# Performance work log

Hardware: AMD Instinct MI355X
Metric: run time of the kernel (lower is better)

The kernel has to match this reference:

```python
import jax, jax.numpy as jnp
import numpy as np
import math

B, H, S, DK = 2, 16, 2048, 64

def setup_inputs() -> dict:
    key = jax.random.key(0)
    kq, kk, kv, km = jax.random.split(key, 4)
    q = jax.random.normal(kq, (B, H, S, DK), dtype=jnp.float32)
    k = jax.random.normal(kk, (B, H, S, DK), dtype=jnp.float32)
    v = jax.random.normal(kv, (B, H, S, DK), dtype=jnp.float32)
    mask = jax.random.randint(km, (1, 1, S, S), 0, 2).astype(jnp.bool_)
    return {"q": q, "k": k, "v": v, "mask": mask}

def reference(q, k, v, mask):
    d_k = q.shape[-1]
    # scores: [B,H,Sq,Sk]
    scores = jnp.einsum('bhqd,bhkd->bhqk', q, k) / math.sqrt(d_k)
    scores = jnp.where(mask, jnp.float32(-1e9), scores)
    # NOTE: original uses nn.Softmax(dim=2) -> softmax over the QUERY axis
    attn = jax.nn.softmax(scores, axis=2)
    out = jnp.einsum('bhqk,bhkd->bhqd', attn, v)
    return out
```

## Files before the change

### kernel.cpp

```cpp
#include <hip/hip_runtime.h>
#include <math.h>

#define S_LEN 2048
#define NCH   32
#define N_BH  32

typedef short bf16x8 __attribute__((ext_vector_type(8)));
typedef _Float16 f16x8 __attribute__((ext_vector_type(8)));
typedef __fp16 fp16x2 __attribute__((ext_vector_type(2)));
typedef float f32x4  __attribute__((ext_vector_type(4)));
typedef unsigned short u16;
typedef unsigned short u16x8 __attribute__((ext_vector_type(8)));
typedef unsigned long long u64;

#define MFMA32(a,b,c) __builtin_amdgcn_mfma_f32_16x16x32_bf16((a),(b),(c),0,0,0)
#define MFMAH(a,b,c)  __builtin_amdgcn_mfma_f32_16x16x32_f16((a),(b),(c),0,0,0)
#define EXP2(x) __builtin_amdgcn_exp2f(x)

#define SC        0.18033688011112042f
#define MASKED_P  6.103515625e-05f

__device__ __forceinline__ u16 f2h(float x) {
  union { _Float16 h; u16 u; } v;
  v.h = (_Float16)x;
  return v.u;
}
__device__ __forceinline__ u16 f2bf_rne(float x) {
  unsigned u = __float_as_uint(x);
  return (u16)((u + 0x7FFF + ((u >> 16) & 1)) >> 16);
}
__device__ __forceinline__ void bfsplit(float x, u16& h, u16& l) {
  unsigned u = __float_as_uint(x);
  h = (u16)(u >> 16);
  float hf = __uint_as_float(u & 0xFFFF0000u);
  l = f2bf_rne(x - hf);
}

__global__ __launch_bounds__(256) void pack_mask(
    const int* __restrict__ mask, u64* __restrict__ bits) {
  const int word = blockIdx.x * 4 + (threadIdx.x >> 6);
  const int lane = threadIdx.x & 63;
  const int row = word >> 5, wc = word & 31;
  int m = mask[(size_t)row * S_LEN + wc * 64 + lane];
  u64 b = __ballot(m != 0);
  if (lane == 0) bits[word] = b;
}

__global__ __launch_bounds__(256) void prep_qk_mask(
    const float* __restrict__ Q, const float* __restrict__ K,
    const int* __restrict__ mask,
    u16* __restrict__ qf, u16* __restrict__ kf, u64* __restrict__ bits) {
  const int b = blockIdx.x;
  const int tid = threadIdx.x;
  if (b < 1024) {
    const int slot = tid & 15, r0 = tid >> 4;
    const size_t rowbase = (size_t)b * 64;
#pragma unroll
    for (int p = 0; p < 4; ++p) {
      const size_t row = rowbase + p * 16 + r0;
      const size_t dst = row * 64 + ((slot * 4) ^ (((int)row & 7) << 3));
      float4 xq = *(const float4*)(Q + row * 64 + slot * 4);
      *(ushort4*)(qf + dst) = make_ushort4(
          f2h(xq.x * SC), f2h(xq.y * SC), f2h(xq.z * SC), f2h(xq.w * SC));
      float4 xk = *(const float4*)(K + row * 64 + slot * 4);
      *(ushort4*)(kf + dst) = make_ushort4(
          f2h(xk.x), f2h(xk.y), f2h(xk.z), f2h(xk.w));
    }
  } else {
    const int word = (b - 1024) * 4 + (tid >> 6);
    const int lane = tid & 63;
    const int row = word >> 5, wc = word & 31;
    int m = mask[(size_t)row * S_LEN + wc * 64 + lane];
    u64 bb = __ballot(m != 0);
    if (lane == 0) bits[word] = bb;
  }
}

__global__ __launch_bounds__(256) void prep_w(
    const float* __restrict__ V, const float* __restrict__ part,
    u16* __restrict__ w_t) {
  __shared__ __align__(16) u16 ts[4096];
  const int tid = threadIdx.x;
  const int kc = blockIdx.x, bh = blockIdx.y;
  const int k = tid >> 2, dblk = (tid & 3) * 16;
  const size_t ko = (size_t)bh * S_LEN + kc * 64 + k;
  const float lsum = part[ko] + part[65536 + ko]
                   + part[131072 + ko] + part[196608 + ko];
  const float ilk = 1.0f / lsum;
  const float* vb = V + ko * 64 + dblk;
#pragma unroll
  for (int u = 0; u < 4; ++u) {
    float4 x = *(const float4*)(vb + u * 4);
    float xs[4] = {x.x, x.y, x.z, x.w};
#pragma unroll
    for (int e = 0; e < 4; ++e) {
      const int d = dblk + u * 4 + e;
      ts[d * 64 + (k ^ ((d & 7) << 3))] = f2h(xs[e] * ilk);
    }
  }
  __syncthreads();
  u16* dst = w_t + ((size_t)bh * NCH + kc) * 4096;
#pragma unroll
  for (int j = 0; j < 2; ++j)
    *(u16x8*)(dst + j * 2048 + tid * 8) = *(const u16x8*)(ts + j * 2048 + tid * 8);
}

__global__ __launch_bounds__(512, 4) void passA(
    const u16* __restrict__ qf, const u16* __restrict__ kf,
    const u64* __restrict__ mbits, float* __restrict__ part) {
  __shared__ __align__(16) u16 qbuf[2][4096];

  const int tid = threadIdx.x;
  const int lane = tid & 63;
  const int w = tid >> 6;
  const int c = lane & 15;
  const int g = lane >> 4;
  const int bx = blockIdx.x;
  const int bh = blockIdx.y;
  const int qp = blockIdx.z;

  const size_t bh_off = (size_t)bh * S_LEN * 64;
  const int swc = (c & 7) << 3;

  f16x8 ka[2][2];
#pragma unroll
  for (int t = 0; t < 2; ++t) {
    const int row = bx * 256 + w * 32 + t * 16 + c;
#pragma unroll
    for (int h = 0; h < 2; ++h)
      ka[t][h] = *(const f16x8*)(kf + bh_off + (size_t)row * 64
                                 + ((h * 32 + g * 8) ^ swc));
  }

  u16x8 stg = *(const u16x8*)(qf + bh_off + (size_t)(qp * 512) * 64 + tid * 8);
  *(u16x8*)(&qbuf[0][0] + tid * 8) = stg;
  __syncthreads();

  float lp[2][4] = {{0.f, 0.f, 0.f, 0.f}, {0.f, 0.f, 0.f, 0.f}};
  const int word = bx * 4 + (w >> 1);
  const int sh0 = (w & 1) * 32;

  int cur = 0;
  for (int qs = 0; qs < 8; ++qs) {
    if (qs + 1 < 8)
      stg = *(const u16x8*)(qf + bh_off
            + (size_t)(qp * 512 + (qs + 1) * 64) * 64 + tid * 8);

    const u16* qb = &qbuf[cur][0];
#pragma unroll
    for (int sub = 0; sub < 4; ++sub) {
      f16x8 fh[2];
      const int rb = sub * 1024 + c * 64;
#pragma unroll
      for (int h = 0; h < 2; ++h)
        fh[h] = *(const f16x8*)(qb + rb + ((h * 32 + g * 8) ^ swc));
      const int qrow = qp * 512 + qs * 64 + sub * 16 + c;
      const u64 mw = mbits[(size_t)qrow * NCH + word];
#pragma unroll
      for (int t = 0; t < 2; ++t) {
        f32x4 acc = {0.f, 0.f, 0.f, 0.f};
        __builtin_amdgcn_s_setprio(1);
        acc = MFMAH(ka[t][0], fh[0], acc);
        acc = MFMAH(ka[t][1], fh[1], acc);
        __builtin_amdgcn_s_setprio(0);
        const unsigned nib = (unsigned)(mw >> (sh0 + t * 16 + g * 4)) & 0xFu;
#pragma unroll
        for (int r = 0; r < 4; ++r) {
          const float tv = EXP2(acc[r]);
          lp[t][r] += ((nib >> r) & 1) ? MASKED_P : tv;
        }
      }
    }

    if (qs + 1 < 8)
      *(u16x8*)(&qbuf[cur ^ 1][0] + tid * 8) = stg;
    __syncthreads();
    cur ^= 1;
  }

#pragma unroll
  for (int off = 1; off < 16; off <<= 1)
#pragma unroll
    for (int t = 0; t < 2; ++t)
#pragma unroll
      for (int r = 0; r < 4; ++r) lp[t][r] += __shfl_xor(lp[t][r], off, 64);
  if (c == 0) {
#pragma unroll
    for (int t = 0; t < 2; ++t) {
      float4 o = {lp[t][0], lp[t][1], lp[t][2], lp[t][3]};
      *(float4*)(part + (size_t)qp * 65536 + (size_t)bh * S_LEN
                 + bx * 256 + w * 32 + t * 16 + g * 4) = o;
    }
  }
}

__global__ __launch_bounds__(256, 4) void passC(
    const u16* __restrict__ qf, const u16* __restrict__ kf,
    const u16* __restrict__ w_t, const u64* __restrict__ mbits,
    float* __restrict__ out) {
  __shared__ __align__(16) u16 sbuf[2][8192];
  __shared__ __align__(16) u16 p_s[4096];

  const int tid = threadIdx.x;
  const int lane = tid & 63;
  const int w = tid >> 6;
  const int c = lane & 15;
  const int g = lane >> 4;
  const int qc = blockIdx.x;
  const int bh = blockIdx.y;

  const size_t bh_off = (size_t)bh * S_LEN * 64;
  const u16* tb_k = kf + bh_off;
  const u16* tb_w = w_t + (size_t)bh * NCH * 4096;
  const int swc = (c & 7) << 3;

  const int qrow = qc * 64 + w * 16 + c;
  f16x8 qb_[2];
#pragma unroll
  for (int h = 0; h < 2; ++h)
    qb_[h] = *(const f16x8*)(qf + bh_off + (size_t)qrow * 64
                             + ((h * 32 + g * 8) ^ swc));

  f32x4 oacc[4];
#pragma unroll
  for (int dt = 0; dt < 4; ++dt) oacc[dt] = (f32x4){0.f, 0.f, 0.f, 0.f};

  const int pbase = w * 1024 + c * 64;
  const int so = tid * 8;

  u16x8 stg[4];
#pragma unroll
  for (int j = 0; j < 2; ++j) {
    stg[0 + j] = *(const u16x8*)(tb_k + j * 2048 + so);
    stg[2 + j] = *(const u16x8*)(tb_w + j * 2048 + so);
  }
#pragma unroll
  for (int j = 0; j < 2; ++j) {
    *(u16x8*)(&sbuf[0][0] + j * 2048 + so) = stg[0 + j];
    *(u16x8*)(&sbuf[0][0] + 4096 + j * 2048 + so) = stg[2 + j];
  }
  __syncthreads();

  int cur = 0;
  for (int kc = 0; kc < NCH; ++kc) {
    if (kc + 1 < NCH) {
      const size_t nb = (size_t)(kc + 1) * 4096;
#pragma unroll
      for (int j = 0; j < 2; ++j) {
        stg[0 + j] = *(const u16x8*)(tb_k + nb + j * 2048 + so);
        stg[2 + j] = *(const u16x8*)(tb_w + nb + j * 2048 + so);
      }
    }

    const u16* bufc = &sbuf[cur][0];
    const u64 mw = mbits[(size_t)qrow * NCH + kc];

#pragma unroll
    for (int kt = 0; kt < 4; ++kt) {
      const int kbase = (16 * kt + c) * 64;
      f16x8 ak0 = *(const f16x8*)(bufc + kbase + ((g * 8) ^ swc));
      f16x8 ak1 = *(const f16x8*)(bufc + kbase + ((32 + g * 8) ^ swc));
      f32x4 acc = {0.f, 0.f, 0.f, 0.f};
      __builtin_amdgcn_s_setprio(1);
      acc = MFMAH(ak0, qb_[0], acc);
      acc = MFMAH(ak1, qb_[1], acc);
      __builtin_amdgcn_s_setprio(0);
      const unsigned nib = (unsigned)(mw >> (kt * 16 + g * 4)) & 0xFu;
      float p[4];
#pragma unroll
      for (int r = 0; r < 4; ++r) {
        const float tv = EXP2(acc[r]);
        p[r] = ((nib >> r) & 1) ? MASKED_P : tv;
      }
      union { fp16x2 h; unsigned u; } cl, ch;
      cl.h = __builtin_amdgcn_cvt_pkrtz(p[0], p[1]);
      ch.h = __builtin_amdgcn_cvt_pkrtz(p[2], p[3]);
      *(uint2*)(p_s + pbase + ((kt * 16 + g * 4) ^ swc)) = make_uint2(cl.u, ch.u);
    }

    __builtin_amdgcn_s_setprio(1);
#pragma unroll
    for (int s2 = 0; s2 < 2; ++s2) {
      const int koff = (s2 * 32 + g * 8) ^ swc;
      f16x8 pb8 = *(const f16x8*)(p_s + pbase + koff);
#pragma unroll
      for (int dt = 0; dt < 4; ++dt) {
        f16x8 av = *(const f16x8*)(bufc + 4096 + (16 * dt + c) * 64 + koff);
        oacc[dt] = MFMAH(av, pb8, oacc[dt]);
      }
    }
    __builtin_amdgcn_s_setprio(0);

    if (kc + 1 < NCH) {
      u16* bufn = &sbuf[cur ^ 1][0];
#pragma unroll
      for (int j = 0; j < 2; ++j) {
        *(u16x8*)(bufn + j * 2048 + so) = stg[0 + j];
        *(u16x8*)(bufn + 4096 + j * 2048 + so) = stg[2 + j];
      }
    }
    __syncthreads();
    cur ^= 1;
  }

  float* ob = out + (bh_off + (size_t)qrow * 64);
#pragma unroll
  for (int dt = 0; dt < 4; ++dt) {
    float4 o = {oacc[dt][0], oacc[dt][1], oacc[dt][2], oacc[dt][3]};
    *(float4*)(ob + dt * 16 + g * 4) = o;
  }
}

__global__ __launch_bounds__(256) void passA_colsum(
    const float* __restrict__ Q, const float* __restrict__ K,
    const u64* __restrict__ mbits, float* __restrict__ il_out) {
  const int tid = threadIdx.x;
  const int lane = tid & 63;
  const int w = tid >> 6;
  const int c = lane & 15;
  const int g = lane >> 4;
  const int kc = blockIdx.x;
  const int bh = blockIdx.y;

  const float* Qb = Q + (size_t)bh * S_LEN * 64;
  const float* Kb = K + (size_t)bh * S_LEN * 64;

  bf16x8 kah[2], kal[2];
  {
    const int krow = kc * 64 + w * 16 + c;
#pragma unroll
    for (int h = 0; h < 2; ++h) {
      const float* src = Kb + (size_t)krow * 64 + h * 32 + g * 8;
      float4 x = *(const float4*)(src);
      float4 y = *(const float4*)(src + 4);
      float xs[8] = {x.x, x.y, x.z, x.w, y.x, y.y, y.z, y.w};
#pragma unroll
      for (int e = 0; e < 8; ++e) {
        u16 hh, ll; bfsplit(xs[e], hh, ll);
        kah[h][e] = (short)hh; kal[h][e] = (short)ll;
      }
    }
  }

  float lp[4] = {0.f, 0.f, 0.f, 0.f};
  const int shift = w * 16 + g * 4;

  for (int qs = 0; qs < S_LEN / 16; ++qs) {
    const int qrow = qs * 16 + c;
    bf16x8 qbh_[2], qbl_[2];
#pragma unroll
    for (int h = 0; h < 2; ++h) {
      const float* src = Qb + (size_t)qrow * 64 + h * 32 + g * 8;
      float4 x = *(const float4*)(src);
      float4 y = *(const float4*)(src + 4);
      float xs[8] = {x.x, x.y, x.z, x.w, y.x, y.y, y.z, y.w};
#pragma unroll
      for (int e = 0; e < 8; ++e) {
        u16 hh, ll; bfsplit(xs[e] * SC, hh, ll);
        qbh_[h][e] = (short)hh; qbl_[h][e] = (short)ll;
      }
    }
    f32x4 acc = {0.f, 0.f, 0.f, 0.f};
#pragma unroll
    for (int h = 0; h < 2; ++h) {
      acc = MFMA32(kah[h], qbh_[h], acc);
      acc = MFMA32(kal[h], qbh_[h], acc);
      acc = MFMA32(kah[h], qbl_[h], acc);
    }
    u64 mw = mbits[(size_t)qrow * NCH + kc];
    unsigned nib = (unsigned)(mw >> shift) & 0xFu;
#pragma unroll
    for (int r = 0; r < 4; ++r) {
      float s = ((nib >> r) & 1) ? -30.0f : acc[r];
      lp[r] += exp2f(s);
    }
  }
#pragma unroll
  for (int off = 1; off < 16; off <<= 1)
#pragma unroll
    for (int r = 0; r < 4; ++r) lp[r] += __shfl_xor(lp[r], off, 64);
  if (c == 0) {
    float4 o = {1.f / lp[0], 1.f / lp[1], 1.f / lp[2], 1.f / lp[3]};
    *(float4*)(il_out + (size_t)bh * S_LEN + kc * 64 + w * 16 + g * 4) = o;
  }
}

__global__ __launch_bounds__(256) void passC_out(
    const float* __restrict__ Q, const float* __restrict__ K,
    const float* __restrict__ V, const u64* __restrict__ mbits,
    const float* __restrict__ il_in, float* __restrict__ out) {
  __shared__ u16 kh_s[4096];
  __shared__ u16 kl_s[4096];
  __shared__ u16 vt_s[4096];
  __shared__ u16 p_s[4096];

  const int tid = threadIdx.x;
  const int lane = tid & 63;
  const int w = tid >> 6;
  const int c = lane & 15;
  const int g = lane >> 4;
  const int qc = blockIdx.x;
  const int bh = blockIdx.y;

  const float* Qb = Q + (size_t)bh * S_LEN * 64;
  const float* Kb = K + (size_t)bh * S_LEN * 64;
  const float* Vb = V + (size_t)bh * S_LEN * 64;

  bf16x8 qbh_[2], qbl_[2];
  {
    const int qrow = qc * 64 + w * 16 + c;
#pragma unroll
    for (int h = 0; h < 2; ++h) {
      const float* src = Qb + (size_t)qrow * 64 + h * 32 + g * 8;
      float4 x = *(const float4*)(src);
      float4 y = *(const float4*)(src + 4);
      float xs[8] = {x.x, x.y, x.z, x.w, y.x, y.y, y.z, y.w};
#pragma unroll
      for (int e = 0; e < 8; ++e) {
        u16 hh, ll; bfsplit(xs[e] * SC, hh, ll);
        qbh_[h][e] = (short)hh; qbl_[h][e] = (short)ll;
      }
    }
  }

  f32x4 oacc[4];
#pragma unroll
  for (int dt = 0; dt < 4; ++dt) oacc[dt] = (f32x4){0.f, 0.f, 0.f, 0.f};

  const int slot = tid & 15, r0 = tid >> 4;
  const int kv = tid & 63, dblk = tid >> 6;
  const int swc = (c & 7) << 3;
  const int pbase = w * 1024 + c * 64;

  for (int kc = 0; kc < NCH; ++kc) {
    __syncthreads();
#pragma unroll
    for (int p = 0; p < 4; ++p) {
      const int row = p * 16 + r0;
      float4 kx = *(const float4*)(Kb + (size_t)(kc * 64 + row) * 64 + slot * 4);
      float xs[4] = {kx.x, kx.y, kx.z, kx.w};
      u16 ha[4], la[4];
#pragma unroll
      for (int e = 0; e < 4; ++e) bfsplit(xs[e], ha[e], la[e]);
      const int idx = row * 64 + ((slot * 4) ^ ((row & 7) << 3));
      *(ushort4*)(kh_s + idx) = make_ushort4(ha[0], ha[1], ha[2], ha[3]);
      *(ushort4*)(kl_s + idx) = make_ushort4(la[0], la[1], la[2], la[3]);
    }
    {
      const float ilk = il_in[(size_t)bh * S_LEN + kc * 64 + kv];
#pragma unroll
      for (int u = 0; u < 4; ++u) {
        float4 vv = *(const float4*)(Vb + (size_t)(kc * 64 + kv) * 64 + dblk * 16 + u * 4);
        float xs[4] = {vv.x, vv.y, vv.z, vv.w};
#pragma unroll
        for (int e = 0; e < 4; ++e) {
          const int d = dblk * 16 + u * 4 + e;
          vt_s[d * 64 + (kv ^ ((d & 7) << 3))] = f2bf_rne(xs[e] * ilk);
        }
      }
    }
    __syncthreads();

    const u64 mw = mbits[(size_t)(qc * 64 + w * 16 + c) * NCH + kc];

#pragma unroll
    for (int kt = 0; kt < 4; ++kt) {
      const int kbase = (16 * kt + c) * 64;
      bf16x8 akh[2], akl[2];
#pragma unroll
      for (int h = 0; h < 2; ++h) {
        const int off = (h * 32 + g * 8) ^ swc;
        akh[h] = *(const bf16x8*)(kh_s + kbase + off);
        akl[h] = *(const bf16x8*)(kl_s + kbase + off);
      }
      f32x4 acc = {0.f, 0.f, 0.f, 0.f};
#pragma unroll
      for (int h = 0; h < 2; ++h) {
        acc = MFMA32(akh[h], qbh_[h], acc);
        acc = MFMA32(akl[h], qbh_[h], acc);
        acc = MFMA32(akh[h], qbl_[h], acc);
      }
      const unsigned nib = (unsigned)(mw >> (kt * 16 + g * 4)) & 0xFu;
      u16 pb[4];
#pragma unroll
      for (int r = 0; r < 4; ++r) {
        const float s = ((nib >> r) & 1) ? -30.0f : acc[r];
        pb[r] = f2bf_rne(exp2f(s));
      }
      *(ushort4*)(p_s + pbase + ((kt * 16 + g * 4) ^ swc)) =
          make_ushort4(pb[0], pb[1], pb[2], pb[3]);
    }
    __syncthreads();

#pragma unroll
    for (int s = 0; s < 2; ++s) {
      const int koff = (s * 32 + 8 * g) ^ swc;
      bf16x8 pb8 = *(const bf16x8*)(p_s + pbase + koff);
#pragma unroll
      for (int dt = 0; dt < 4; ++dt) {
        bf16x8 av = *(const bf16x8*)(vt_s + (16 * dt + c) * 64 + koff);
        oacc[dt] = MFMA32(av, pb8, oacc[dt]);
      }
    }
  }

  float* ob = out + ((size_t)bh * S_LEN + qc * 64 + w * 16 + c) * 64;
#pragma unroll
  for (int dt = 0; dt < 4; ++dt) {
    float4 o = {oacc[dt][0], oacc[dt][1], oacc[dt][2], oacc[dt][3]};
    *(float4*)(ob + dt * 16 + g * 4) = o;
  }
}

extern "C" void kernel_launch(void* const* d_in, const int* in_sizes, int n_in,
                              void* d_out, int out_size, void* d_ws, size_t ws_size,
                              hipStream_t stream) {
  (void)in_sizes; (void)n_in; (void)out_size;
  const float* q = (const float*)d_in[0];
  const float* k = (const float*)d_in[1];
  const float* v = (const float*)d_in[2];
  const int* mask = (const int*)d_in[3];
  float* out = (float*)d_out;

  u64* mbits = (u64*)d_ws;
  float* part = (float*)((char*)d_ws + 524288);
  const size_t PL = (size_t)N_BH * S_LEN * 64;
  u16* qf = (u16*)((char*)d_ws + 524288 + 1048576);
  u16* kf = qf + PL;
  u16* w_t = kf + PL;
  const size_t need = 524288 + 1048576 + 3 * PL * sizeof(u16);

  if (ws_size >= need) {
    prep_qk_mask<<<dim3(1024 + S_LEN * NCH / 4), 256, 0, stream>>>(
        q, k, mask, qf, kf, mbits);
    passA<<<dim3(8, N_BH, 4), 512, 0, stream>>>(qf, kf, mbits, part);
    prep_w<<<dim3(NCH, N_BH), 256, 0, stream>>>(v, part, w_t);
    passC<<<dim3(NCH, N_BH), 256, 0, stream>>>(qf, kf, w_t, mbits, out);
  } else {
    pack_mask<<<dim3(S_LEN * NCH / 4), 256, 0, stream>>>(mask, mbits);
    float* il = part;
    dim3 grid(NCH, N_BH);
    passA_colsum<<<grid, 256, 0, stream>>>(q, k, mbits, il);
    passC_out<<<grid, 256, 0, stream>>>(q, k, v, mbits, il, out);
  }
}
```

Baseline: 124.8 us.

## Keep P in registers and use 16x16x16 MFMA with permuted V layout

Removes the shared-memory round trip for the probability tile in passC. Each lane's exp results now stay in registers as f16x4 fragments and feed 16x16x16 f16 MFMAs directly. To match that operand layout, prep_w writes the transposed, scaled V tile in a permuted, swizzled order, so each 8-element read splits into two K=16 halves. This saves LDS traffic and a store/load dependency, but doubles the MFMA instruction count with smaller, lower-throughput ops, and drops the setprio hints.

```diff
diff --git a/kernel.cpp b/kernel.cpp
--- a/kernel.cpp
+++ b/kernel.cpp
@@ -7,7 +7,7 @@
 
 typedef short bf16x8 __attribute__((ext_vector_type(8)));
 typedef _Float16 f16x8 __attribute__((ext_vector_type(8)));
-typedef __fp16 fp16x2 __attribute__((ext_vector_type(2)));
+typedef _Float16 f16x4 __attribute__((ext_vector_type(4)));
 typedef float f32x4  __attribute__((ext_vector_type(4)));
 typedef unsigned short u16;
 typedef unsigned short u16x8 __attribute__((ext_vector_type(8)));
@@ -16,6 +16,17 @@
 #define MFMA32(a,b,c) __builtin_amdgcn_mfma_f32_16x16x32_bf16((a),(b),(c),0,0,0)
 #define MFMAH(a,b,c)  __builtin_amdgcn_mfma_f32_16x16x32_f16((a),(b),(c),0,0,0)
 #define EXP2(x) __builtin_amdgcn_exp2f(x)
+
+__device__ __forceinline__ f32x4 mfma16(f16x4 a, f16x4 b, f32x4 c) {
+#if __has_builtin(__builtin_amdgcn_mfma_f32_16x16x16f16)
+  return __builtin_amdgcn_mfma_f32_16x16x16f16(a, b, c, 0, 0, 0);
+#else
+  const _Float16 z = (_Float16)0.0f;
+  f16x8 a8 = {a[0], a[1], a[2], a[3], z, z, z, z};
+  f16x8 b8 = {b[0], b[1], b[2], b[3], z, z, z, z};
+  return MFMAH(a8, b8, c);
+#endif
+}
 
 #define SC        0.18033688011112042f
 #define MASKED_P  6.103515625e-05f
@@ -83,6 +94,9 @@
   const int tid = threadIdx.x;
   const int kc = blockIdx.x, bh = blockIdx.y;
   const int k = tid >> 2, dblk = (tid & 3) * 16;
+  const int kt = k >> 4, gg = (k >> 2) & 3, r = k & 3;
+  const int sub = (kt & 1) * 4 + r;
+  const int lu = gg * 2 + (kt >> 1);
   const size_t ko = (size_t)bh * S_LEN + kc * 64 + k;
   const float lsum = part[ko] + part[65536 + ko]
                    + part[131072 + ko] + part[196608 + ko];
@@ -95,7 +109,7 @@
 #pragma unroll
     for (int e = 0; e < 4; ++e) {
       const int d = dblk + u * 4 + e;
-      ts[d * 64 + (k ^ ((d & 7) << 3))] = f2h(xs[e] * ilk);
+      ts[d * 64 + (((lu ^ (d & 7)) << 3) + sub)] = f2h(xs[e] * ilk);
     }
   }
   __syncthreads();
@@ -199,7 +213,6 @@
     const u16* __restrict__ w_t, const u64* __restrict__ mbits,
     float* __restrict__ out) {
   __shared__ __align__(16) u16 sbuf[2][8192];
-  __shared__ __align__(16) u16 p_s[4096];
 
   const int tid = threadIdx.x;
   const int lane = tid & 63;
@@ -225,7 +238,6 @@
 #pragma unroll
   for (int dt = 0; dt < 4; ++dt) oacc[dt] = (f32x4){0.f, 0.f, 0.f, 0.f};
 
-  const int pbase = w * 1024 + c * 64;
   const int so = tid * 8;
 
   u16x8 stg[4];
@@ -255,41 +267,36 @@
     const u16* bufc = &sbuf[cur][0];
     const u64 mw = mbits[(size_t)qrow * NCH + kc];
 
+    f16x4 pf[4];
 #pragma unroll
     for (int kt = 0; kt < 4; ++kt) {
       const int kbase = (16 * kt + c) * 64;
       f16x8 ak0 = *(const f16x8*)(bufc + kbase + ((g * 8) ^ swc));
       f16x8 ak1 = *(const f16x8*)(bufc + kbase + ((32 + g * 8) ^ swc));
       f32x4 acc = {0.f, 0.f, 0.f, 0.f};
-      __builtin_amdgcn_s_setprio(1);
       acc = MFMAH(ak0, qb_[0], acc);
       acc = MFMAH(ak1, qb_[1], acc);
-      __builtin_amdgcn_s_setprio(0);
       const unsigned nib = (unsigned)(mw >> (kt * 16 + g * 4)) & 0xFu;
-      float p[4];
 #pragma unroll
       for (int r = 0; r < 4; ++r) {
         const float tv = EXP2(acc[r]);
-        p[r] = ((nib >> r) & 1) ? MASKED_P : tv;
-      }
-      union { fp16x2 h; unsigned u; } cl, ch;
-      cl.h = __builtin_amdgcn_cvt_pkrtz(p[0], p[1]);
-      ch.h = __builtin_amdgcn_cvt_pkrtz(p[2], p[3]);
-      *(uint2*)(p_s + pbase + ((kt * 16 + g * 4) ^ swc)) = make_uint2(cl.u, ch.u);
-    }
-
-    __builtin_amdgcn_s_setprio(1);
-#pragma unroll
-    for (int s2 = 0; s2 < 2; ++s2) {
-      const int koff = (s2 * 32 + g * 8) ^ swc;
-      f16x8 pb8 = *(const f16x8*)(p_s + pbase + koff);
+        pf[kt][r] = (_Float16)(((nib >> r) & 1) ? MASKED_P : tv);
+      }
+    }
+
+#pragma unroll
+    for (int ktp = 0; ktp < 2; ++ktp) {
 #pragma unroll
       for (int dt = 0; dt < 4; ++dt) {
-        f16x8 av = *(const f16x8*)(bufc + 4096 + (16 * dt + c) * 64 + koff);
-        oacc[dt] = MFMAH(av, pb8, oacc[dt]);
-      }
-    }
-    __builtin_amdgcn_s_setprio(0);
+        const int aoff = 4096 + (16 * dt + c) * 64
+                       + (((g * 2 + ktp) ^ (c & 7)) << 3);
+        f16x8 av = *(const f16x8*)(bufc + aoff);
+        f16x4 alo = {av[0], av[1], av[2], av[3]};
+        f16x4 ahi = {av[4], av[5], av[6], av[7]};
+        oacc[dt] = mfma16(alo, pf[ktp * 2], oacc[dt]);
+        oacc[dt] = mfma16(ahi, pf[ktp * 2 + 1], oacc[dt]);
+      }
+    }
 
     if (kc + 1 < NCH) {
       u16* bufn = &sbuf[cur ^ 1][0];
```

New measurement: 124.4 us (median of 2 runs). No clear change (-0.4%).
